# Kernel optimization log

Measured on AMD Instinct MI355X. Metric: run time of the kernel, lower is better.

Reference implementation:

```python
import jax, jax.numpy as jnp
import numpy as np

N = 50000   # nodes
E = 600000  # edges
D = 128     # in/out features


def setup_inputs() -> dict:
    key = jax.random.key(0)
    k1, k2, k3, k4, k5, k6 = jax.random.split(key, 6)
    input = jax.random.normal(k1, (N, D), dtype=jnp.float32)
    W = jax.random.normal(k2, (D, D), dtype=jnp.float32) * (1.0 / np.sqrt(D))
    b = jax.random.normal(k3, (D,), dtype=jnp.float32) * 0.01
    adj_row = jnp.sort(jax.random.randint(k4, (E,), 0, N, dtype=jnp.int32))
    adj_col = jax.random.randint(k5, (E,), 0, N, dtype=jnp.int32)
    adj_val = jax.random.uniform(k6, (E,), dtype=jnp.float32)
    return {"input": input, "W": W, "b": b,
            "adj_row": adj_row, "adj_col": adj_col, "adj_val": adj_val}


def reference(input, W, b, adj_row, adj_col, adj_val):
    # support = Linear(input)  -> [N, D]
    support = jnp.einsum('nd,od->no', input, W) + b
    # sparse adj (COO) @ support : gather source rows, scale by edge value,
    # scatter-add into destination rows.
    msgs = support[adj_col] * adj_val[:, None]           # [E, D]
    agg = jax.ops.segment_sum(msgs, adj_row, num_segments=input.shape[0])
    return jnp.tanh(agg)
```

## Files before the change

kernel.cpp:

```cpp
#include <hip/hip_runtime.h>
#include <hip/hip_fp16.h>
#include <cmath>

#define DF 128
#define WPITCHH 136

typedef _Float16 f16x8 __attribute__((ext_vector_type(8)));
typedef _Float16 f16x4 __attribute__((ext_vector_type(4)));
typedef float    f32x4 __attribute__((ext_vector_type(4)));

__global__ __launch_bounds__(256)
void gemm_mfma_kernel(const float* __restrict__ X, const _Float16* __restrict__ Wh,
                      const float* __restrict__ bias, __half* __restrict__ S,
                      int N)
{
    __shared__ _Float16 Wl[DF * WPITCHH];

    const int t    = threadIdx.x;
    const int lane = t & 63;
    const int l15  = lane & 15;
    const int q    = lane >> 4;
    const int m0   = (blockIdx.x * 4 + (t >> 6)) * 16;

    #pragma unroll
    for (int l = 0; l < 8; ++l) {
        int flat = l * 256 + t;
        int r    = flat >> 4;
        int c8   = (flat & 15) * 8;
        f16x8 v = *(const f16x8*)(Wh + (size_t)r * DF + c8);
        *(f16x8*)(Wl + r * WPITCHH + c8) = v;
    }
    __syncthreads();
    if (m0 >= N) return;

    f32x4 acc[8];
    #pragma unroll
    for (int nt = 0; nt < 8; ++nt) acc[nt] = (f32x4){0.f, 0.f, 0.f, 0.f};

    const int xrow = min(m0 + l15, N - 1);
    #pragma unroll
    for (int kc = 0; kc < DF; kc += 32) {
        const float* xp = X + (size_t)xrow * DF + kc + q * 8;
        float4 xa = *(const float4*)xp;
        float4 xb = *(const float4*)(xp + 4);
        f16x8 A;
        A[0] = (_Float16)xa.x; A[1] = (_Float16)xa.y;
        A[2] = (_Float16)xa.z; A[3] = (_Float16)xa.w;
        A[4] = (_Float16)xb.x; A[5] = (_Float16)xb.y;
        A[6] = (_Float16)xb.z; A[7] = (_Float16)xb.w;
        #pragma unroll
        for (int nt = 0; nt < 8; ++nt) {
            f16x8 B = *(const f16x8*)(Wl + (nt * 16 + l15) * WPITCHH + kc + q * 8);
            acc[nt] = __builtin_amdgcn_mfma_f32_16x16x32_f16(B, A, acc[nt], 0, 0, 0);
        }
    }

    const int mrow = m0 + l15;
    if (mrow < N) {
        _Float16* rowp = (_Float16*)S + (size_t)mrow * DF;
        #pragma unroll
        for (int nt = 0; nt < 8; ++nt) {
            float4 bv = *(const float4*)(bias + nt * 16 + q * 4);
            f16x4 hv;
            hv[0] = (_Float16)(acc[nt][0] + bv.x);
            hv[1] = (_Float16)(acc[nt][1] + bv.y);
            hv[2] = (_Float16)(acc[nt][2] + bv.z);
            hv[3] = (_Float16)(acc[nt][3] + bv.w);
            *(f16x4*)(rowp + nt * 16 + q * 4) = hv;
        }
    }
}

__global__ __launch_bounds__(256)
void build_meta_kernel(const int* __restrict__ arow, const int* __restrict__ acol,
                       const float* __restrict__ aval, const float* __restrict__ W,
                       int* __restrict__ rowptr, int2* __restrict__ pk,
                       _Float16* __restrict__ Wh, int N, int E)
{
    int e = blockIdx.x * 256 + threadIdx.x;
    if (e >= E) return;
    if (e < DF * DF) Wh[e] = (_Float16)W[e];
    pk[e] = make_int2(acol[e] << 8, __float_as_int(aval[e]));
    int r = arow[e];
    int rprev = (e == 0) ? -1 : arow[e - 1];
    for (int n = rprev + 1; n <= r; ++n) rowptr[n] = e;
    if (e == E - 1) {
        for (int n = r + 1; n <= N; ++n) rowptr[n] = E;
    }
}

__global__ __launch_bounds__(256)
void agg_tanh_kernel(const __half* __restrict__ S, const int* __restrict__ rowptr,
                     const int2* __restrict__ pk, float* __restrict__ out, int Nn)
{
    const int n  = (blockIdx.x * 256 + threadIdx.x) >> 4;
    if (n >= Nn) return;
    const int f  = threadIdx.x & 15;
    const int fb = f * 16;

    const int start = rowptr[n];
    const int end   = rowptr[n + 1];
    const char* Sb  = (const char*)S;

    float acc[8];
    #pragma unroll
    for (int i = 0; i < 8; ++i) acc[i] = 0.f;

    int e = start;
    for (; e + 8 <= end; e += 8) {
        int2 p[8];
        #pragma unroll
        for (int u = 0; u < 8; ++u) p[u] = pk[e + u];
        f16x8 h[8];
        #pragma unroll
        for (int u = 0; u < 8; ++u)
            h[u] = *(const f16x8*)(Sb + (size_t)(unsigned)p[u].x + fb);
        #pragma unroll
        for (int u = 0; u < 8; ++u) {
            const float v = __int_as_float(p[u].y);
            #pragma unroll
            for (int i = 0; i < 8; ++i) acc[i] += (float)h[u][i] * v;
        }
    }
    if (e + 4 <= end) {
        int2 p[4];
        #pragma unroll
        for (int u = 0; u < 4; ++u) p[u] = pk[e + u];
        f16x8 h[4];
        #pragma unroll
        for (int u = 0; u < 4; ++u)
            h[u] = *(const f16x8*)(Sb + (size_t)(unsigned)p[u].x + fb);
        #pragma unroll
        for (int u = 0; u < 4; ++u) {
            const float v = __int_as_float(p[u].y);
            #pragma unroll
            for (int i = 0; i < 8; ++i) acc[i] += (float)h[u][i] * v;
        }
        e += 4;
    }
    for (; e < end; ++e) {
        int2 p = pk[e];
        f16x8 h = *(const f16x8*)(Sb + (size_t)(unsigned)p.x + fb);
        const float v = __int_as_float(p.y);
        #pragma unroll
        for (int i = 0; i < 8; ++i) acc[i] += (float)h[i] * v;
    }

    float4 o0, o1;
    o0.x = tanhf(acc[0]); o0.y = tanhf(acc[1]);
    o0.z = tanhf(acc[2]); o0.w = tanhf(acc[3]);
    o1.x = tanhf(acc[4]); o1.y = tanhf(acc[5]);
    o1.z = tanhf(acc[6]); o1.w = tanhf(acc[7]);
    float* op = out + (size_t)n * DF + f * 8;
    *(float4*)op       = o0;
    *(float4*)(op + 4) = o1;
}

extern "C" void kernel_launch(void* const* d_in, const int* in_sizes, int n_in,
                              void* d_out, int out_size, void* d_ws, size_t ws_size,
                              hipStream_t stream)
{
    const float* X    = (const float*)d_in[0];
    const float* W    = (const float*)d_in[1];
    const float* bias = (const float*)d_in[2];
    const int*   arow = (const int*)  d_in[3];
    const int*   acol = (const int*)  d_in[4];
    const float* aval = (const float*)d_in[5];
    float* out = (float*)d_out;

    const int N = in_sizes[0] / DF;
    const int E = in_sizes[3];

    __half*   S      = (__half*)d_ws;
    _Float16* Wh     = (_Float16*)((char*)d_ws + (size_t)N * DF * sizeof(__half));
    int*      rowptr = (int*)((char*)Wh + (size_t)DF * DF * sizeof(_Float16));
    int2*     pk     = (int2*)(rowptr + (N + 2));

    build_meta_kernel<<<(E + 255) / 256, 256, 0, stream>>>(arow, acol, aval, W,
                                                           rowptr, pk, Wh, N, E);

    gemm_mfma_kernel<<<(N + 63) / 64, 256, 0, stream>>>(X, Wh, bias, S, N);

    agg_tanh_kernel<<<(N * 16 + 255) / 256, 256, 0, stream>>>(S, rowptr, pk, out, N);
}
```

Baseline: 125.8 us.

## Pad per-row edge lists to multiples of eight and fuse rowptr build into GEMM

The GEMM kernel now converts W to fp16 directly while staging it into shared memory, and extra blocks in the same launch build the CSR row pointer. A new kernel writes the packed edge records into a layout where each row is padded to a multiple of eight with zero-weight entries. This lets the aggregation kernel use only the eight-wide unrolled loop with no remainder paths. The padding adds memory and extra gathers of row 0, and the edge-packing pass still runs as a separate dependent kernel launch.

```diff
diff --git a/kernel.cpp b/kernel.cpp
--- a/kernel.cpp
+++ b/kernel.cpp
@@ -10,13 +10,27 @@
 typedef float    f32x4 __attribute__((ext_vector_type(4)));
 
 __global__ __launch_bounds__(256)
-void gemm_mfma_kernel(const float* __restrict__ X, const _Float16* __restrict__ Wh,
+void gemm_meta_kernel(const float* __restrict__ X, const float* __restrict__ W,
                       const float* __restrict__ bias, __half* __restrict__ S,
-                      int N)
+                      const int* __restrict__ arow, int* __restrict__ rowptr,
+                      int N, int E, int GB)
 {
     __shared__ _Float16 Wl[DF * WPITCHH];
 
-    const int t    = threadIdx.x;
+    const int t = threadIdx.x;
+
+    if (blockIdx.x >= GB) {
+        int e = (blockIdx.x - GB) * 256 + t;
+        if (e >= E) return;
+        int r = arow[e];
+        int rprev = (e == 0) ? -1 : arow[e - 1];
+        for (int n = rprev + 1; n <= r; ++n) rowptr[n] = e;
+        if (e == E - 1) {
+            for (int n = r + 1; n <= N; ++n) rowptr[n] = E;
+        }
+        return;
+    }
+
     const int lane = t & 63;
     const int l15  = lane & 15;
     const int q    = lane >> 4;
@@ -27,7 +41,14 @@
         int flat = l * 256 + t;
         int r    = flat >> 4;
         int c8   = (flat & 15) * 8;
-        f16x8 v = *(const f16x8*)(Wh + (size_t)r * DF + c8);
+        const float* wp = W + (size_t)r * DF + c8;
+        float4 wa = *(const float4*)wp;
+        float4 wb = *(const float4*)(wp + 4);
+        f16x8 v;
+        v[0] = (_Float16)wa.x; v[1] = (_Float16)wa.y;
+        v[2] = (_Float16)wa.z; v[3] = (_Float16)wa.w;
+        v[4] = (_Float16)wb.x; v[5] = (_Float16)wb.y;
+        v[6] = (_Float16)wb.z; v[7] = (_Float16)wb.w;
         *(f16x8*)(Wl + r * WPITCHH + c8) = v;
     }
     __syncthreads();
@@ -72,26 +93,30 @@
 }
 
 __global__ __launch_bounds__(256)
-void build_meta_kernel(const int* __restrict__ arow, const int* __restrict__ acol,
-                       const float* __restrict__ aval, const float* __restrict__ W,
-                       int* __restrict__ rowptr, int2* __restrict__ pk,
-                       _Float16* __restrict__ Wh, int N, int E)
+void build_epk_kernel(const int* __restrict__ arow, const int* __restrict__ acol,
+                      const float* __restrict__ aval, const int* __restrict__ rowptr,
+                      int2* __restrict__ epk, int N, int E)
 {
-    int e = blockIdx.x * 256 + threadIdx.x;
-    if (e >= E) return;
-    if (e < DF * DF) Wh[e] = (_Float16)W[e];
-    pk[e] = make_int2(acol[e] << 8, __float_as_int(aval[e]));
-    int r = arow[e];
-    int rprev = (e == 0) ? -1 : arow[e - 1];
-    for (int n = rprev + 1; n <= r; ++n) rowptr[n] = e;
-    if (e == E - 1) {
-        for (int n = r + 1; n <= N; ++n) rowptr[n] = E;
+    int tid = blockIdx.x * 256 + threadIdx.x;
+    if (tid < E) {
+        int n    = arow[tid];
+        int base = rowptr[n];
+        int s2   = (base + 8 * n + 7) & ~7;
+        epk[s2 + (tid - base)] = make_int2(acol[tid] << 8, __float_as_int(aval[tid]));
+    }
+    if (tid < N) {
+        int start = rowptr[tid];
+        int end   = rowptr[tid + 1];
+        int cnt   = end - start;
+        int s2    = (start + 8 * tid + 7) & ~7;
+        int cpad  = (cnt + 7) & ~7;
+        for (int k = cnt; k < cpad; ++k) epk[s2 + k] = make_int2(0, 0);
     }
 }
 
 __global__ __launch_bounds__(256)
 void agg_tanh_kernel(const __half* __restrict__ S, const int* __restrict__ rowptr,
-                     const int2* __restrict__ pk, float* __restrict__ out, int Nn)
+                     const int2* __restrict__ epk, float* __restrict__ out, int Nn)
 {
     const int n  = (blockIdx.x * 256 + threadIdx.x) >> 4;
     if (n >= Nn) return;
@@ -99,18 +124,19 @@
     const int fb = f * 16;
 
     const int start = rowptr[n];
-    const int end   = rowptr[n + 1];
+    const int cnt   = rowptr[n + 1] - start;
+    const int s2    = (start + 8 * n + 7) & ~7;
     const char* Sb  = (const char*)S;
 
     float acc[8];
     #pragma unroll
     for (int i = 0; i < 8; ++i) acc[i] = 0.f;
 
-    int e = start;
-    for (; e + 8 <= end; e += 8) {
+    for (int b = 0; b < cnt; b += 8) {
+        const int2* pp = epk + s2 + b;
         int2 p[8];
         #pragma unroll
-        for (int u = 0; u < 8; ++u) p[u] = pk[e + u];
+        for (int u = 0; u < 8; ++u) p[u] = pp[u];
         f16x8 h[8];
         #pragma unroll
         for (int u = 0; u < 8; ++u)
@@ -121,29 +147,6 @@
             #pragma unroll
             for (int i = 0; i < 8; ++i) acc[i] += (float)h[u][i] * v;
         }
-    }
-    if (e + 4 <= end) {
-        int2 p[4];
-        #pragma unroll
-        for (int u = 0; u < 4; ++u) p[u] = pk[e + u];
-        f16x8 h[4];
-        #pragma unroll
-        for (int u = 0; u < 4; ++u)
-            h[u] = *(const f16x8*)(Sb + (size_t)(unsigned)p[u].x + fb);
-        #pragma unroll
-        for (int u = 0; u < 4; ++u) {
-            const float v = __int_as_float(p[u].y);
-            #pragma unroll
-            for (int i = 0; i < 8; ++i) acc[i] += (float)h[u][i] * v;
-        }
-        e += 4;
-    }
-    for (; e < end; ++e) {
-        int2 p = pk[e];
-        f16x8 h = *(const f16x8*)(Sb + (size_t)(unsigned)p.x + fb);
-        const float v = __int_as_float(p.y);
-        #pragma unroll
-        for (int i = 0; i < 8; ++i) acc[i] += (float)h[i] * v;
     }
 
     float4 o0, o1;
@@ -171,15 +174,18 @@
     const int N = in_sizes[0] / DF;
     const int E = in_sizes[3];
 
-    __half*   S      = (__half*)d_ws;
-    _Float16* Wh     = (_Float16*)((char*)d_ws + (size_t)N * DF * sizeof(__half));
-    int*      rowptr = (int*)((char*)Wh + (size_t)DF * DF * sizeof(_Float16));
-    int2*     pk     = (int2*)(rowptr + (N + 2));
+    __half* S      = (__half*)d_ws;
+    int*    rowptr = (int*)((char*)d_ws + (size_t)N * DF * sizeof(__half));
+    int2*   epk    = (int2*)(rowptr + (N + 2));
 
-    build_meta_kernel<<<(E + 255) / 256, 256, 0, stream>>>(arow, acol, aval, W,
-                                                           rowptr, pk, Wh, N, E);
+    const int GB = (N + 63) / 64;
+    const int MB = (E + 255) / 256;
 
-    gemm_mfma_kernel<<<(N + 63) / 64, 256, 0, stream>>>(X, Wh, bias, S, N);
+    gemm_meta_kernel<<<GB + MB, 256, 0, stream>>>(X, W, bias, S, arow, rowptr,
+                                                  N, E, GB);
 
-    agg_tanh_kernel<<<(N * 16 + 255) / 256, 256, 0, stream>>>(S, rowptr, pk, out, N);
+    build_epk_kernel<<<(E + 255) / 256, 256, 0, stream>>>(arow, acol, aval,
+                                                          rowptr, epk, N, E);
+
+    agg_tanh_kernel<<<(N * 16 + 255) / 256, 256, 0, stream>>>(S, rowptr, epk, out, N);
 }
```

New measurement: 125.4 us. About the same (-0.3%).

## Merge metadata build into GEMM launch and convert W in-kernel

Applied to the files above, without the earlier changes.

Folds the CSR/packed-edge build into the GEMM launch as extra blocks and converts W from fp32 to fp16 directly while staging it into LDS, which removes one kernel launch and the Wh workspace. The goal is to cut launch overhead and let the metadata work run alongside the GEMM. A new fdot2-based aggregation kernel is added but never launched, and it writes no real output. The launched aggregation kernel is the renamed original.

```diff
diff --git a/kernel.cpp b/kernel.cpp
--- a/kernel.cpp
+++ b/kernel.cpp
@@ -7,16 +7,34 @@
 
 typedef _Float16 f16x8 __attribute__((ext_vector_type(8)));
 typedef _Float16 f16x4 __attribute__((ext_vector_type(4)));
+typedef _Float16 f16x2 __attribute__((ext_vector_type(2)));
 typedef float    f32x4 __attribute__((ext_vector_type(4)));
 
 __global__ __launch_bounds__(256)
-void gemm_mfma_kernel(const float* __restrict__ X, const _Float16* __restrict__ Wh,
-                      const float* __restrict__ bias, __half* __restrict__ S,
-                      int N)
+void gemm_meta_kernel(const float* __restrict__ X, const float* __restrict__ W,
+                      const float* __restrict__ bias, _Float16* __restrict__ S,
+                      const int* __restrict__ arow, const int* __restrict__ acol,
+                      const float* __restrict__ aval,
+                      int* __restrict__ rowptr, int2* __restrict__ pk,
+                      int N, int E, int GB)
 {
     __shared__ _Float16 Wl[DF * WPITCHH];
 
-    const int t    = threadIdx.x;
+    const int t = threadIdx.x;
+
+    if (blockIdx.x >= GB) {
+        int e = (blockIdx.x - GB) * 256 + t;
+        if (e >= E) return;
+        pk[e] = make_int2(acol[e] << 8, __float_as_int(aval[e]));
+        int r = arow[e];
+        int rprev = (e == 0) ? -1 : arow[e - 1];
+        for (int n = rprev + 1; n <= r; ++n) rowptr[n] = e;
+        if (e == E - 1) {
+            for (int n = r + 1; n <= N; ++n) rowptr[n] = E;
+        }
+        return;
+    }
+
     const int lane = t & 63;
     const int l15  = lane & 15;
     const int q    = lane >> 4;
@@ -27,7 +45,14 @@
         int flat = l * 256 + t;
         int r    = flat >> 4;
         int c8   = (flat & 15) * 8;
-        f16x8 v = *(const f16x8*)(Wh + (size_t)r * DF + c8);
+        const float* wp = W + (size_t)r * DF + c8;
+        float4 wa = *(const float4*)wp;
+        float4 wb = *(const float4*)(wp + 4);
+        f16x8 v;
+        v[0] = (_Float16)wa.x; v[1] = (_Float16)wa.y;
+        v[2] = (_Float16)wa.z; v[3] = (_Float16)wa.w;
+        v[4] = (_Float16)wb.x; v[5] = (_Float16)wb.y;
+        v[6] = (_Float16)wb.z; v[7] = (_Float16)wb.w;
         *(f16x8*)(Wl + r * WPITCHH + c8) = v;
     }
     __syncthreads();
@@ -57,7 +82,7 @@
 
     const int mrow = m0 + l15;
     if (mrow < N) {
-        _Float16* rowp = (_Float16*)S + (size_t)mrow * DF;
+        _Float16* rowp = S + (size_t)mrow * DF;
         #pragma unroll
         for (int nt = 0; nt < 8; ++nt) {
             float4 bv = *(const float4*)(bias + nt * 16 + q * 4);
@@ -72,26 +97,87 @@
 }
 
 __global__ __launch_bounds__(256)
-void build_meta_kernel(const int* __restrict__ arow, const int* __restrict__ acol,
-                       const float* __restrict__ aval, const float* __restrict__ W,
-                       int* __restrict__ rowptr, int2* __restrict__ pk,
-                       _Float16* __restrict__ Wh, int N, int E)
-{
-    int e = blockIdx.x * 256 + threadIdx.x;
-    if (e >= E) return;
-    if (e < DF * DF) Wh[e] = (_Float16)W[e];
-    pk[e] = make_int2(acol[e] << 8, __float_as_int(aval[e]));
-    int r = arow[e];
-    int rprev = (e == 0) ? -1 : arow[e - 1];
-    for (int n = rprev + 1; n <= r; ++n) rowptr[n] = e;
-    if (e == E - 1) {
-        for (int n = r + 1; n <= N; ++n) rowptr[n] = E;
-    }
+void agg_tanh_kernel(const _Float16* __restrict__ S, const int* __restrict__ rowptr,
+                     const int2* __restrict__ pk, float* __restrict__ out, int Nn)
+{
+    const int n  = (blockIdx.x * 256 + threadIdx.x) >> 4;
+    if (n >= Nn) return;
+    const int f  = threadIdx.x & 15;
+    const int fb = f * 16;
+
+    const int start = rowptr[n];
+    const int end   = rowptr[n + 1];
+    const char* Sb  = (const char*)S;
+
+    float acc[4];
+    #pragma unroll
+    for (int i = 0; i < 4; ++i) acc[i] = 0.f;
+
+    int e = start;
+    for (; e + 8 <= end; e += 8) {
+        int2 p[8];
+        #pragma unroll
+        for (int u = 0; u < 8; ++u) p[u] = pk[e + u];
+        f16x8 h[8];
+        #pragma unroll
+        for (int u = 0; u < 8; ++u)
+            h[u] = *(const f16x8*)(Sb + (size_t)(unsigned)p[u].x + fb);
+        #pragma unroll
+        for (int u = 0; u < 8; ++u) {
+            const _Float16 vh = (_Float16)__int_as_float(p[u].y);
+            f16x2 vv; vv[0] = vh; vv[1] = vh;
+            #pragma unroll
+            for (int i = 0; i < 4; ++i) {
+                f16x2 hp; hp[0] = h[u][2 * i]; hp[1] = h[u][2 * i + 1];
+                acc[i] = __builtin_amdgcn_fdot2(hp, vv, acc[i], false);
+            }
+        }
+    }
+    if (e + 4 <= end) {
+        int2 p[4];
+        #pragma unroll
+        for (int u = 0; u < 4; ++u) p[u] = pk[e + u];
+        f16x8 h[4];
+        #pragma unroll
+        for (int u = 0; u < 4; ++u)
+            h[u] = *(const f16x8*)(Sb + (size_t)(unsigned)p[u].x + fb);
+        #pragma unroll
+        for (int u = 0; u < 4; ++u) {
+            const _Float16 vh = (_Float16)__int_as_float(p[u].y);
+            f16x2 vv; vv[0] = vh; vv[1] = vh;
+            #pragma unroll
+            for (int i = 0; i < 4; ++i) {
+                f16x2 hp; hp[0] = h[u][2 * i]; hp[1] = h[u][2 * i + 1];
+                acc[i] = __builtin_amdgcn_fdot2(hp, vv, acc[i], false);
+            }
+        }
+        e += 4;
+    }
+    for (; e < end; ++e) {
+        int2 p = pk[e];
+        f16x8 h = *(const f16x8*)(Sb + (size_t)(unsigned)p.x + fb);
+        const _Float16 vh = (_Float16)__int_as_float(p.y);
+        f16x2 vv; vv[0] = vh; vv[1] = vh;
+        #pragma unroll
+        for (int i = 0; i < 4; ++i) {
+            f16x2 hp; hp[0] = h[2 * i]; hp[1] = h[2 * i + 1];
+            acc[i] = __builtin_amdgcn_fdot2(hp, vv, acc[i], false);
+        }
+    }
+
+
+    float4 dummy; (void)dummy;
+
+    out[0] = out[0];
+    float o[8];
+    #pragma unroll
+    for (int i = 0; i < 4; ++i) { o[2 * i] = acc[i]; o[2 * i + 1] = 0.f; }
+    (void)o;
 }
 
 __global__ __launch_bounds__(256)
-void agg_tanh_kernel(const __half* __restrict__ S, const int* __restrict__ rowptr,
-                     const int2* __restrict__ pk, float* __restrict__ out, int Nn)
+void agg_tanh_safe_kernel(const _Float16* __restrict__ S, const int* __restrict__ rowptr,
+                          const int2* __restrict__ pk, float* __restrict__ out, int Nn)
 {
     const int n  = (blockIdx.x * 256 + threadIdx.x) >> 4;
     if (n >= Nn) return;
@@ -171,15 +257,16 @@
     const int N = in_sizes[0] / DF;
     const int E = in_sizes[3];
 
-    __half*   S      = (__half*)d_ws;
-    _Float16* Wh     = (_Float16*)((char*)d_ws + (size_t)N * DF * sizeof(__half));
-    int*      rowptr = (int*)((char*)Wh + (size_t)DF * DF * sizeof(_Float16));
+    _Float16* S      = (_Float16*)d_ws;
+    int*      rowptr = (int*)((char*)d_ws + (size_t)N * DF * sizeof(_Float16));
     int2*     pk     = (int2*)(rowptr + (N + 2));
 
-    build_meta_kernel<<<(E + 255) / 256, 256, 0, stream>>>(arow, acol, aval, W,
-                                                           rowptr, pk, Wh, N, E);
-
-    gemm_mfma_kernel<<<(N + 63) / 64, 256, 0, stream>>>(X, Wh, bias, S, N);
-
-    agg_tanh_kernel<<<(N * 16 + 255) / 256, 256, 0, stream>>>(S, rowptr, pk, out, N);
-}
+    const int GB = (N + 63) / 64;
+    const int MB = (E + 255) / 256;
+
+    gemm_meta_kernel<<<GB + MB, 256, 0, stream>>>(X, W, bias, S, arow, acol,
+                                                  aval, rowptr, pk, N, E, GB);
+
+    agg_tanh_safe_kernel<<<(N * 16 + 255) / 256, 256, 0, stream>>>(S, rowptr,
+                                                                   pk, out, N);
+}
```

New measurement: 124.2 us. No clear change (-1.3%).
